# Performance work log

Measured on AMD Instinct MI355X. Metric: run time of the kernel, lower is better.

## Reference

```python
import jax, jax.numpy as jnp
import numpy as np

HIDDEN = 1024
NUM_HEADS = 16
HEAD_DIM = HIDDEN // NUM_HEADS


def setup_inputs() -> dict:
    key = jax.random.key(0)
    ks = jax.random.split(key, 9)
    B, S, Hs = 2, 2048, HIDDEN
    scale = 1.0 / np.sqrt(Hs)
    inp = {
        "hidden_state": jax.random.normal(ks[0], (B, S, Hs), dtype=jnp.float32),
        # causal mask, exactly (B, num_heads, S, S) as the module's assert requires
        "attention_mask": jnp.broadcast_to(
            jnp.tril(jnp.ones((S, S), dtype=bool)), (B, NUM_HEADS, S, S)
        ),
        "wq": jax.random.normal(ks[1], (Hs, Hs), dtype=jnp.float32) * scale,
        "bq": jnp.zeros((Hs,), dtype=jnp.float32),
        "wk": jax.random.normal(ks[2], (Hs, Hs), dtype=jnp.float32) * scale,
        "bk": jnp.zeros((Hs,), dtype=jnp.float32),
        "wv": jax.random.normal(ks[3], (Hs, Hs), dtype=jnp.float32) * scale,
        "bv": jnp.zeros((Hs,), dtype=jnp.float32),
        "wo": jax.random.normal(ks[4], (Hs, Hs), dtype=jnp.float32) * scale,
        "bo": jnp.zeros((Hs,), dtype=jnp.float32),
    }
    return inp


def _split_heads(x):
    B, S, _ = x.shape
    return x.reshape(B, S, NUM_HEADS, HEAD_DIM).transpose(0, 2, 1, 3)  # (B,H,S,D)


def reference(hidden_state, attention_mask, wq, bq, wk, bk, wv, bv, wo, bo):
    B, S, Hs = hidden_state.shape
    # torch nn.Linear: x @ W.T + b
    q = _split_heads(hidden_state @ wq.T + bq)
    k = _split_heads(hidden_state @ wk.T + bk)
    v = _split_heads(hidden_state @ wv.T + bv)
    scores = jnp.einsum("bhsd,bhtd->bhst", q, k) / jnp.sqrt(
        jnp.asarray(HEAD_DIM, dtype=jnp.float32)
    )
    scores = jnp.where(attention_mask, scores, -jnp.inf)
    probs = jax.nn.softmax(scores, axis=-1)
    # dropout p=0.0 (eval/deterministic) -> identity
    out = jnp.einsum("bhst,bhtd->bhsd", probs, v)
    out = out.transpose(0, 2, 1, 3).reshape(B, S, Hs)
    return out @ wo.T + bo
```

## Files before the change

### kernel.cpp

```cpp
#include <hip/hip_runtime.h>
#include <stdint.h>
#include <stddef.h>


typedef __attribute__((ext_vector_type(8))) short short8;
typedef __attribute__((ext_vector_type(4))) float f32x4;
typedef __attribute__((ext_vector_type(4))) unsigned int u32x4;
typedef __attribute__((ext_vector_type(2))) unsigned int u32x2;
typedef __attribute__((ext_vector_type(4))) unsigned short u16x4;

static __device__ __forceinline__ unsigned short f2bf(float f){
  union { float f; unsigned u; } v; v.f = f;
  unsigned r = v.u + 0x7FFFu + ((v.u >> 16) & 1u);
  return (unsigned short)(r >> 16);
}
static __device__ __forceinline__ unsigned pk2bf(float lo, float hi){
  return (unsigned)f2bf(lo) | ((unsigned)f2bf(hi) << 16);
}

static __device__ __forceinline__ void gl_lds16(const void* g, void* l){
  __builtin_amdgcn_global_load_lds((const __attribute__((address_space(1))) void*)g,
                                   (__attribute__((address_space(3))) void*)l, 16, 0, 0);
}

__global__ __launch_bounds__(256) void k_cvt_all(const float* __restrict__ X,
                                                 const float* __restrict__ w0, const float* __restrict__ w1,
                                                 const float* __restrict__ w2, const float* __restrict__ w3,
                                                 unsigned short* __restrict__ Xb,
                                                 unsigned short* __restrict__ Wb){
  int bid = blockIdx.x;
  const float* src; unsigned short* dst; int i;
  if (bid < 4096){ src = X; dst = Xb; i = bid*256 + threadIdx.x; }
  else {
    int w = (bid - 4096) >> 10;
    const float* srcs[4] = {w0,w1,w2,w3};
    src = srcs[w]; dst = Wb + (size_t)w*1048576u;
    i = ((bid - 4096) & 1023)*256 + threadIdx.x;
  }
  f32x4 x = ((const f32x4*)src)[i];
  u16x4 y = { f2bf(x[0]), f2bf(x[1]), f2bf(x[2]), f2bf(x[3]) };
  ((u16x4*)dst)[i] = y;
}

template<int MODE, int MT>
__global__ __launch_bounds__(256) void k_gemm_bt(
    const unsigned short* __restrict__ A,
    const unsigned short* __restrict__ B,
    const float* __restrict__ bias0, const float* __restrict__ bias1, const float* __restrict__ bias2,
    void* __restrict__ Cout, unsigned short* __restrict__ Vt, int N, int K)
{
  static_assert(MT==64 || MT==128, "MT");
  constexpr int I  = MT/32;
  constexpr int NA = MT/64;
  __shared__ unsigned short lds_a[MT*32];
  __shared__ unsigned short lds_b[128*32];
  const int t = threadIdx.x;
  const int lane = t & 63, wave = t >> 6;
  const int wy = wave >> 1, wx = wave & 1;
  const int m0 = blockIdx.y * MT, n0 = blockIdx.x * 128;
  const int mrow = lane & 15, quad = lane >> 4;
  const unsigned short* ga = A + (size_t)(m0 + (t>>2)) * K + (t&3)*8;
  const unsigned short* gb = B + (size_t)(n0 + (t>>2)) * K + (t&3)*8;
  char* la = (char*)lds_a + wave*1024;
  char* lb = (char*)lds_b + wave*1024;

  f32x4 acc[I][4];
  #pragma unroll
  for (int i=0;i<I;i++)
    #pragma unroll
    for (int j=0;j<4;j++) acc[i][j] = (f32x4){0.f,0.f,0.f,0.f};

  for (int k0=0;k0<K;k0+=32){
    __syncthreads();
    #pragma unroll
    for (int p=0;p<NA;p++) gl_lds16(ga + (size_t)p*64*K + k0, la + p*4096);
    #pragma unroll
    for (int p=0;p<2;p++)  gl_lds16(gb + (size_t)p*64*K + k0, lb + p*4096);
    __syncthreads();
    short8 af[I], bf[4];
    #pragma unroll
    for (int i=0;i<I;i++) af[i] = *(const short8*)(lds_a + (wy*(MT/2)+i*16+mrow)*32 + quad*8);
    #pragma unroll
    for (int j=0;j<4;j++) bf[j] = *(const short8*)(lds_b + (wx*64+j*16+mrow)*32 + quad*8);
    #pragma unroll
    for (int i=0;i<I;i++)
      #pragma unroll
      for (int j=0;j<4;j++)
        acc[i][j] = __builtin_amdgcn_mfma_f32_16x16x32_bf16(af[i], bf[j], acc[i][j], 0,0,0);
  }

  const bool vblk = (MODE==0) && (n0 >= 2048);
  #pragma unroll
  for (int j=0;j<4;j++){
    int col = n0 + wx*64 + j*16 + mrow;
    float bv;
    if (MODE==0){
      int cb = col >> 10;
      const float* bp = (cb==0)?bias0:((cb==1)?bias1:bias2);
      bv = bp[col & 1023];
    } else {
      bv = bias0[col];
    }
    #pragma unroll
    for (int i=0;i<I;i++){
      int rbase = m0 + wy*(MT/2) + i*16 + quad*4;
      if (vblk){
        int bh = (rbase >> 11) * 16 + ((col >> 6) & 15);
        unsigned short* vp = Vt + ((size_t)bh*64 + (col & 63))*2048 + (rbase & 2047);
        u32x2 w = { pk2bf(acc[i][0 ][0], 0.f) };
        (void)w;
        u32x2 wv = { pk2bf(acc[i][j][0]+bv, acc[i][j][1]+bv),
                     pk2bf(acc[i][j][2]+bv, acc[i][j][3]+bv) };
        *(u32x2*)vp = wv;
      } else {
        #pragma unroll
        for (int r=0;r<4;r++){
          float v = acc[i][j][r] + bv;
          if (MODE==1) ((float*)Cout)[(size_t)(rbase+r)*N + col] = v;
          else         ((unsigned short*)Cout)[(size_t)(rbase+r)*N + col] = f2bf(v);
        }
      }
    }
  }
}

__global__ __launch_bounds__(256) void k_attn(const unsigned short* __restrict__ QKV,
                                              const unsigned short* __restrict__ Vt,
                                              unsigned short* __restrict__ Ctx){
  __shared__ unsigned short lds_k[64*72];
  __shared__ unsigned short lds_v[64*72];
  __shared__ unsigned short lds_p[4][16*72];
  const int t = threadIdx.x;
  const int lane = t & 63, wave = t >> 6;
  const int mrow = lane & 15, quad = lane >> 4;
  const int bh = blockIdx.y, b = bh >> 4, h = bh & 15;
  const int qt = (bh & 16) ? (15 - blockIdx.x) : blockIdx.x;
  const int q0 = qt * 128;
  const size_t qkvbase = (size_t)b*2048*3072 + (size_t)h*64;
  const float C1 = 0.125f * 1.44269504f;
  const float C0 = -16.f  * 1.44269504f;

  short8 qf[2][2];
  #pragma unroll
  for (int qh=0;qh<2;qh++){
    const unsigned short* qp = QKV + qkvbase + (size_t)(q0 + qh*64 + wave*16 + mrow) * 3072;
    qf[qh][0] = *(const short8*)(qp + quad*8);
    qf[qh][1] = *(const short8*)(qp + 32 + quad*8);
  }
  float l_i[2] = {0.f, 0.f};
  f32x4 oacc[2][4];
  #pragma unroll
  for (int qh=0;qh<2;qh++)
    #pragma unroll
    for (int c=0;c<4;c++) oacc[qh][c] = (f32x4){0.f,0.f,0.f,0.f};

  const int njt = 2*qt + 2;
  const unsigned short* kbase = QKV + qkvbase + 1024;
  const unsigned short* vbase = Vt + (size_t)bh*64*2048;
  const int sr = t >> 3, sc = (t & 7) * 8;

  for (int jt=0;jt<njt;jt++){
    const int j0 = jt*64;
    __syncthreads();
    #pragma unroll
    for (int p=0;p<2;p++){
      int r = sr + p*32;
      *(u32x4*)(lds_k + r*72 + sc) = *(const u32x4*)(kbase + (size_t)(j0+r)*3072 + sc);
      *(u32x4*)(lds_v + r*72 + sc) = *(const u32x4*)(vbase + (size_t)r*2048 + j0 + sc);
    }
    __syncthreads();

    #pragma unroll
    for (int qh=0;qh<2;qh++){
      if (qh==0 && jt==njt-1) continue;
      const int grow = q0 + qh*64 + wave*16 + mrow;

      f32x4 sacc[4];
      #pragma unroll
      for (int jb=0;jb<4;jb++) sacc[jb] = (f32x4){0.f,0.f,0.f,0.f};
      #pragma unroll
      for (int jb=0;jb<4;jb++)
        #pragma unroll
        for (int kk=0;kk<2;kk++){
          short8 kf = *(const short8*)(lds_k + (jb*16+mrow)*72 + kk*32 + quad*8);
          sacc[jb] = __builtin_amdgcn_mfma_f32_16x16x32_bf16(kf, qf[qh][kk], sacc[jb], 0,0,0);
        }

      float s[4][4];
      if (jt == 2*qt + qh){
        #pragma unroll
        for (int jb=0;jb<4;jb++){
          int jg = j0 + jb*16 + quad*4;
          #pragma unroll
          for (int r=0;r<4;r++){
            float v = fmaf(sacc[jb][r], C1, C0);
            s[jb][r] = __builtin_amdgcn_exp2f((jg + r <= grow) ? v : -1e30f);
          }
        }
      } else {
        #pragma unroll
        for (int jb=0;jb<4;jb++)
          #pragma unroll
          for (int r=0;r<4;r++)
            s[jb][r] = __builtin_amdgcn_exp2f(fmaf(sacc[jb][r], C1, C0));
      }
      #pragma unroll
      for (int jb=0;jb<4;jb++)
        #pragma unroll
        for (int r=0;r<4;r++) l_i[qh] += s[jb][r];

      unsigned short* pp = lds_p[wave];
      #pragma unroll
      for (int jb=0;jb<4;jb++){
        u32x2 w = { pk2bf(s[jb][0], s[jb][1]), pk2bf(s[jb][2], s[jb][3]) };
        *(u32x2*)(pp + mrow*72 + jb*16 + quad*4) = w;
      }
      __asm__ volatile("s_waitcnt lgkmcnt(0)" ::: "memory");
      short8 pf[2];
      pf[0] = *(const short8*)(pp + mrow*72 + quad*8);
      pf[1] = *(const short8*)(pp + mrow*72 + 32 + quad*8);

      #pragma unroll
      for (int c=0;c<4;c++)
        #pragma unroll
        for (int kk=0;kk<2;kk++){
          short8 vf = *(const short8*)(lds_v + (c*16+mrow)*72 + kk*32 + quad*8);
          oacc[qh][c] = __builtin_amdgcn_mfma_f32_16x16x32_bf16(vf, pf[kk], oacc[qh][c], 0,0,0);
        }
    }
  }

  unsigned short* cp = Ctx + (size_t)b*2048*1024 + (size_t)h*64;
  #pragma unroll
  for (int qh=0;qh<2;qh++){
    float l = l_i[qh];
    l += __shfl_xor(l, 16);
    l += __shfl_xor(l, 32);
    float rl = 1.f / l;
    size_t rowoff = (size_t)(q0 + qh*64 + wave*16 + mrow) * 1024;
    #pragma unroll
    for (int c=0;c<4;c++){
      u32x2 w = { pk2bf(oacc[qh][c][0]*rl, oacc[qh][c][1]*rl),
                  pk2bf(oacc[qh][c][2]*rl, oacc[qh][c][3]*rl) };
      *(u32x2*)(cp + rowoff + c*16 + quad*4) = w;
    }
  }
}

extern "C" void kernel_launch(void* const* d_in, const int* in_sizes, int n_in,
                              void* d_out, int out_size, void* d_ws, size_t ws_size,
                              hipStream_t stream){
  const float* X  = (const float*)d_in[0];
  const float* wq = (const float*)d_in[2];
  const float* bq = (const float*)d_in[3];
  const float* wk = (const float*)d_in[4];
  const float* bk = (const float*)d_in[5];
  const float* wv = (const float*)d_in[6];
  const float* bv = (const float*)d_in[7];
  const float* wo = (const float*)d_in[8];
  const float* bo = (const float*)d_in[9];

  char* ws = (char*)d_ws;
  unsigned short* Xb   = (unsigned short*)(ws);
  unsigned short* Wb   = (unsigned short*)(ws + (8u<<20));
  unsigned short* QKVb = (unsigned short*)(ws + (16u<<20));
  unsigned short* Vt   = (unsigned short*)(ws + (40u<<20));
  unsigned short* Ctxb = (unsigned short*)(ws + (48u<<20));

  k_cvt_all<<<dim3(8192), 256, 0, stream>>>(X, wq, wk, wv, wo, Xb, Wb);
  k_gemm_bt<0,128><<<dim3(24, 32), 256, 0, stream>>>(Xb, Wb, bq, bk, bv, QKVb, Vt, 3072, 1024);
  k_attn<<<dim3(16, 32), 256, 0, stream>>>(QKVb, Vt, Ctxb);
  k_gemm_bt<1,64><<<dim3(8, 64), 256, 0, stream>>>(Ctxb, Wb + 3u*1048576u, bo, bo, bo,
                                                   d_out, nullptr, 1024, 1024);
}
```

Measured before the change: 714.7 us.

## Double-buffer K/V tiles and split query halves across 8 waves in attention

```diff
diff --git a/kernel.cpp b/kernel.cpp
--- a/kernel.cpp
+++ b/kernel.cpp
@@ -107,8 +107,6 @@
       if (vblk){
         int bh = (rbase >> 11) * 16 + ((col >> 6) & 15);
         unsigned short* vp = Vt + ((size_t)bh*64 + (col & 63))*2048 + (rbase & 2047);
-        u32x2 w = { pk2bf(acc[i][0 ][0], 0.f) };
-        (void)w;
         u32x2 wv = { pk2bf(acc[i][j][0]+bv, acc[i][j][1]+bv),
                      pk2bf(acc[i][j][2]+bv, acc[i][j][3]+bv) };
         *(u32x2*)vp = wv;
@@ -124,15 +122,16 @@
   }
 }
 
-__global__ __launch_bounds__(256) void k_attn(const unsigned short* __restrict__ QKV,
-                                              const unsigned short* __restrict__ Vt,
-                                              unsigned short* __restrict__ Ctx){
-  __shared__ unsigned short lds_k[64*72];
-  __shared__ unsigned short lds_v[64*72];
-  __shared__ unsigned short lds_p[4][16*72];
+__global__ __launch_bounds__(512, 4) void k_attn(const unsigned short* __restrict__ QKV,
+                                                 const unsigned short* __restrict__ Vt,
+                                                 unsigned short* __restrict__ Ctx){
+  __shared__ unsigned short lds_k[2][64*72];
+  __shared__ unsigned short lds_v[2][64*72];
+  __shared__ unsigned short lds_p[8][16*72];
   const int t = threadIdx.x;
   const int lane = t & 63, wave = t >> 6;
   const int mrow = lane & 15, quad = lane >> 4;
+  const int qh = wave >> 2;
   const int bh = blockIdx.y, b = bh >> 4, h = bh & 15;
   const int qt = (bh & 16) ? (15 - blockIdx.x) : blockIdx.x;
   const int q0 = qt * 128;
@@ -140,40 +139,44 @@
   const float C1 = 0.125f * 1.44269504f;
   const float C0 = -16.f  * 1.44269504f;
 
-  short8 qf[2][2];
+  const int grow = q0 + wave*16 + mrow;
+  short8 qf[2];
+  {
+    const unsigned short* qp = QKV + qkvbase + (size_t)grow * 3072;
+    qf[0] = *(const short8*)(qp + quad*8);
+    qf[1] = *(const short8*)(qp + 32 + quad*8);
+  }
+  float l_i = 0.f;
+  f32x4 oacc[4];
   #pragma unroll
-  for (int qh=0;qh<2;qh++){
-    const unsigned short* qp = QKV + qkvbase + (size_t)(q0 + qh*64 + wave*16 + mrow) * 3072;
-    qf[qh][0] = *(const short8*)(qp + quad*8);
-    qf[qh][1] = *(const short8*)(qp + 32 + quad*8);
-  }
-  float l_i[2] = {0.f, 0.f};
-  f32x4 oacc[2][4];
-  #pragma unroll
-  for (int qh=0;qh<2;qh++)
-    #pragma unroll
-    for (int c=0;c<4;c++) oacc[qh][c] = (f32x4){0.f,0.f,0.f,0.f};
+  for (int c=0;c<4;c++) oacc[c] = (f32x4){0.f,0.f,0.f,0.f};
 
   const int njt = 2*qt + 2;
+  const int mask_jt = 2*qt + qh;
+  const int skip_jt = (qh==0) ? (njt-1) : -1;
   const unsigned short* kbase = QKV + qkvbase + 1024;
   const unsigned short* vbase = Vt + (size_t)bh*64*2048;
   const int sr = t >> 3, sc = (t & 7) * 8;
 
+  u32x4 kreg = *(const u32x4*)(kbase + (size_t)sr*3072 + sc);
+  u32x4 vreg = *(const u32x4*)(vbase + (size_t)sr*2048 + sc);
+  *(u32x4*)(&lds_k[0][0] + sr*72 + sc) = kreg;
+  *(u32x4*)(&lds_v[0][0] + sr*72 + sc) = vreg;
+
+  int buf = 0;
   for (int jt=0;jt<njt;jt++){
-    const int j0 = jt*64;
     __syncthreads();
-    #pragma unroll
-    for (int p=0;p<2;p++){
-      int r = sr + p*32;
-      *(u32x4*)(lds_k + r*72 + sc) = *(const u32x4*)(kbase + (size_t)(j0+r)*3072 + sc);
-      *(u32x4*)(lds_v + r*72 + sc) = *(const u32x4*)(vbase + (size_t)r*2048 + j0 + sc);
-    }
-    __syncthreads();
-
-    #pragma unroll
-    for (int qh=0;qh<2;qh++){
-      if (qh==0 && jt==njt-1) continue;
-      const int grow = q0 + qh*64 + wave*16 + mrow;
+
+    {
+      const int pj = (jt+1 < njt) ? (jt+1)*64 : 0;
+      kreg = *(const u32x4*)(kbase + (size_t)(pj+sr)*3072 + sc);
+      vreg = *(const u32x4*)(vbase + (size_t)sr*2048 + pj + sc);
+    }
+
+    if (jt != skip_jt){
+      const int j0 = jt*64;
+      const unsigned short* lk = &lds_k[buf][0];
+      const unsigned short* lv = &lds_v[buf][0];
 
       f32x4 sacc[4];
       #pragma unroll
@@ -182,12 +185,12 @@
       for (int jb=0;jb<4;jb++)
         #pragma unroll
         for (int kk=0;kk<2;kk++){
-          short8 kf = *(const short8*)(lds_k + (jb*16+mrow)*72 + kk*32 + quad*8);
-          sacc[jb] = __builtin_amdgcn_mfma_f32_16x16x32_bf16(kf, qf[qh][kk], sacc[jb], 0,0,0);
+          short8 kf = *(const short8*)(lk + (jb*16+mrow)*72 + kk*32 + quad*8);
+          sacc[jb] = __builtin_amdgcn_mfma_f32_16x16x32_bf16(kf, qf[kk], sacc[jb], 0,0,0);
         }
 
       float s[4][4];
-      if (jt == 2*qt + qh){
+      if (jt == mask_jt){
         #pragma unroll
         for (int jb=0;jb<4;jb++){
           int jg = j0 + jb*16 + quad*4;
@@ -207,7 +210,7 @@
       #pragma unroll
       for (int jb=0;jb<4;jb++)
         #pragma unroll
-        for (int r=0;r<4;r++) l_i[qh] += s[jb][r];
+        for (int r=0;r<4;r++) l_i += s[jb][r];
 
       unsigned short* pp = lds_p[wave];
       #pragma unroll
@@ -224,24 +227,27 @@
       for (int c=0;c<4;c++)
         #pragma unroll
         for (int kk=0;kk<2;kk++){
-          short8 vf = *(const short8*)(lds_v + (c*16+mrow)*72 + kk*32 + quad*8);
-          oacc[qh][c] = __builtin_amdgcn_mfma_f32_16x16x32_bf16(vf, pf[kk], oacc[qh][c], 0,0,0);
-        }
-    }
+          short8 vf = *(const short8*)(lv + (c*16+mrow)*72 + kk*32 + quad*8);
+          oacc[c] = __builtin_amdgcn_mfma_f32_16x16x32_bf16(vf, pf[kk], oacc[c], 0,0,0);
+        }
+    }
+
+    *(u32x4*)(&lds_k[buf^1][0] + sr*72 + sc) = kreg;
+    *(u32x4*)(&lds_v[buf^1][0] + sr*72 + sc) = vreg;
+    buf ^= 1;
   }
 
   unsigned short* cp = Ctx + (size_t)b*2048*1024 + (size_t)h*64;
-  #pragma unroll
-  for (int qh=0;qh<2;qh++){
-    float l = l_i[qh];
+  {
+    float l = l_i;
     l += __shfl_xor(l, 16);
     l += __shfl_xor(l, 32);
     float rl = 1.f / l;
-    size_t rowoff = (size_t)(q0 + qh*64 + wave*16 + mrow) * 1024;
+    size_t rowoff = (size_t)grow * 1024;
     #pragma unroll
     for (int c=0;c<4;c++){
-      u32x2 w = { pk2bf(oacc[qh][c][0]*rl, oacc[qh][c][1]*rl),
-                  pk2bf(oacc[qh][c][2]*rl, oacc[qh][c][3]*rl) };
+      u32x2 w = { pk2bf(oacc[c][0]*rl, oacc[c][1]*rl),
+                  pk2bf(oacc[c][2]*rl, oacc[c][3]*rl) };
       *(u32x2*)(cp + rowoff + c*16 + quad*4) = w;
     }
   }
@@ -269,7 +275,7 @@
 
   k_cvt_all<<<dim3(8192), 256, 0, stream>>>(X, wq, wk, wv, wo, Xb, Wb);
   k_gemm_bt<0,128><<<dim3(24, 32), 256, 0, stream>>>(Xb, Wb, bq, bk, bv, QKVb, Vt, 3072, 1024);
-  k_attn<<<dim3(16, 32), 256, 0, stream>>>(QKVb, Vt, Ctxb);
+  k_attn<<<dim3(16, 32), 512, 0, stream>>>(QKVb, Vt, Ctxb);
   k_gemm_bt<1,64><<<dim3(8, 64), 256, 0, stream>>>(Ctxb, Wb + 3u*1048576u, bo, bo, bo,
                                                    d_out, nullptr, 1024, 1024);
 }
```

Result: faster. 696.7 us (-2.5%).

## Double-buffer K/V tiles in attention, keep P in registers, skip masked blocks

Applied to the files above, without the earlier changes.

```diff
diff --git a/kernel.cpp b/kernel.cpp
--- a/kernel.cpp
+++ b/kernel.cpp
@@ -4,11 +4,20 @@
 
 
 typedef __attribute__((ext_vector_type(8))) short short8;
+typedef __attribute__((ext_vector_type(4))) short bf16x4;
 typedef __attribute__((ext_vector_type(4))) float f32x4;
 typedef __attribute__((ext_vector_type(4))) unsigned int u32x4;
 typedef __attribute__((ext_vector_type(2))) unsigned int u32x2;
 typedef __attribute__((ext_vector_type(4))) unsigned short u16x4;
 
+#if __has_builtin(__builtin_amdgcn_mfma_f32_16x16x16bf16_1k)
+  #define MFMA16(a,b,c) __builtin_amdgcn_mfma_f32_16x16x16bf16_1k(a,b,c,0,0,0)
+#elif __has_builtin(__builtin_amdgcn_mfma_f32_16x16x16_bf16)
+  #define MFMA16(a,b,c) __builtin_amdgcn_mfma_f32_16x16x16_bf16(a,b,c,0,0,0)
+#else
+  #define MFMA16(a,b,c) (c)
+#endif
+
 static __device__ __forceinline__ unsigned short f2bf(float f){
   union { float f; unsigned u; } v; v.f = f;
   unsigned r = v.u + 0x7FFFu + ((v.u >> 16) & 1u);
@@ -16,6 +25,11 @@
 }
 static __device__ __forceinline__ unsigned pk2bf(float lo, float hi){
   return (unsigned)f2bf(lo) | ((unsigned)f2bf(hi) << 16);
+}
+static __device__ __forceinline__ unsigned pk2bf_hw(float lo, float hi){
+  unsigned r;
+  asm("v_cvt_pk_bf16_f32 %0, %1, %2" : "=v"(r) : "v"(lo), "v"(hi));
+  return r;
 }
 
 static __device__ __forceinline__ void gl_lds16(const void* g, void* l){
@@ -107,8 +121,6 @@
       if (vblk){
         int bh = (rbase >> 11) * 16 + ((col >> 6) & 15);
         unsigned short* vp = Vt + ((size_t)bh*64 + (col & 63))*2048 + (rbase & 2047);
-        u32x2 w = { pk2bf(acc[i][0 ][0], 0.f) };
-        (void)w;
         u32x2 wv = { pk2bf(acc[i][j][0]+bv, acc[i][j][1]+bv),
                      pk2bf(acc[i][j][2]+bv, acc[i][j][3]+bv) };
         *(u32x2*)vp = wv;
@@ -124,12 +136,11 @@
   }
 }
 
-__global__ __launch_bounds__(256) void k_attn(const unsigned short* __restrict__ QKV,
-                                              const unsigned short* __restrict__ Vt,
-                                              unsigned short* __restrict__ Ctx){
-  __shared__ unsigned short lds_k[64*72];
-  __shared__ unsigned short lds_v[64*72];
-  __shared__ unsigned short lds_p[4][16*72];
+__global__ __launch_bounds__(256, 2) void k_attn(const unsigned short* __restrict__ QKV,
+                                                 const unsigned short* __restrict__ Vt,
+                                                 unsigned short* __restrict__ Ctx){
+  __shared__ unsigned short lds_k[2][128*72];
+  __shared__ unsigned short lds_v[2][64*136];
   const int t = threadIdx.x;
   const int lane = t & 63, wave = t >> 6;
   const int mrow = lane & 15, quad = lane >> 4;
@@ -140,10 +151,11 @@
   const float C1 = 0.125f * 1.44269504f;
   const float C0 = -16.f  * 1.44269504f;
 
-  short8 qf[2][2];
+  int grow2[2]; short8 qf[2][2];
   #pragma unroll
   for (int qh=0;qh<2;qh++){
-    const unsigned short* qp = QKV + qkvbase + (size_t)(q0 + qh*64 + wave*16 + mrow) * 3072;
+    grow2[qh] = q0 + wave*32 + qh*16 + mrow;
+    const unsigned short* qp = QKV + qkvbase + (size_t)grow2[qh] * 3072;
     qf[qh][0] = *(const short8*)(qp + quad*8);
     qf[qh][1] = *(const short8*)(qp + 32 + quad*8);
   }
@@ -154,80 +166,109 @@
     #pragma unroll
     for (int c=0;c<4;c++) oacc[qh][c] = (f32x4){0.f,0.f,0.f,0.f};
 
-  const int njt = 2*qt + 2;
+  const int njt = qt + 1;
   const unsigned short* kbase = QKV + qkvbase + 1024;
   const unsigned short* vbase = Vt + (size_t)bh*64*2048;
-  const int sr = t >> 3, sc = (t & 7) * 8;
-
+
+  u32x4 kreg[4], vreg[4];
+  #pragma unroll
+  for (int p=0;p<4;p++){
+    int c = t + 256*p;
+    kreg[p] = *(const u32x4*)(kbase + (size_t)(c>>3)*3072 + (c&7)*8);
+    vreg[p] = *(const u32x4*)(vbase + (size_t)(c>>4)*2048 + (c&15)*8);
+  }
+  #pragma unroll
+  for (int p=0;p<4;p++){
+    int c = t + 256*p;
+    *(u32x4*)(&lds_k[0][0] + (c>>3)*72  + (c&7)*8)  = kreg[p];
+    *(u32x4*)(&lds_v[0][0] + (c>>4)*136 + (c&15)*8) = vreg[p];
+  }
+
+  int buf = 0;
   for (int jt=0;jt<njt;jt++){
-    const int j0 = jt*64;
     __syncthreads();
-    #pragma unroll
-    for (int p=0;p<2;p++){
-      int r = sr + p*32;
-      *(u32x4*)(lds_k + r*72 + sc) = *(const u32x4*)(kbase + (size_t)(j0+r)*3072 + sc);
-      *(u32x4*)(lds_v + r*72 + sc) = *(const u32x4*)(vbase + (size_t)r*2048 + j0 + sc);
-    }
-    __syncthreads();
-
+
+    {
+      const int pj = (jt+1 < njt) ? (jt+1)*128 : 0;
+      #pragma unroll
+      for (int p=0;p<4;p++){
+        int c = t + 256*p;
+        kreg[p] = *(const u32x4*)(kbase + (size_t)(pj + (c>>3))*3072 + (c&7)*8);
+        vreg[p] = *(const u32x4*)(vbase + (size_t)(c>>4)*2048 + pj + (c&15)*8);
+      }
+    }
+
+    const int j0 = jt*128;
+    const bool diag = (jt == qt);
+    const unsigned short* lk = &lds_k[buf][0];
+    const unsigned short* lv = &lds_v[buf][0];
+
+    f32x4 sacc[2][8];
+    __builtin_amdgcn_s_setprio(1);
+    #pragma unroll
+    for (int jb=0;jb<8;jb++){
+      if (diag && jb > 2*wave+1) continue;
+      short8 kf0 = *(const short8*)(lk + (jb*16+mrow)*72 + quad*8);
+      short8 kf1 = *(const short8*)(lk + (jb*16+mrow)*72 + 32 + quad*8);
+      #pragma unroll
+      for (int qh=0;qh<2;qh++){
+        if (diag && jb > 2*wave+qh) continue;
+        f32x4 a = (f32x4){0.f,0.f,0.f,0.f};
+        a = __builtin_amdgcn_mfma_f32_16x16x32_bf16(kf0, qf[qh][0], a, 0,0,0);
+        a = __builtin_amdgcn_mfma_f32_16x16x32_bf16(kf1, qf[qh][1], a, 0,0,0);
+        sacc[qh][jb] = a;
+      }
+    }
+    __builtin_amdgcn_s_setprio(0);
+
+    unsigned puv[2][8][2];
     #pragma unroll
     for (int qh=0;qh<2;qh++){
-      if (qh==0 && jt==njt-1) continue;
-      const int grow = q0 + qh*64 + wave*16 + mrow;
-
-      f32x4 sacc[4];
-      #pragma unroll
-      for (int jb=0;jb<4;jb++) sacc[jb] = (f32x4){0.f,0.f,0.f,0.f};
-      #pragma unroll
-      for (int jb=0;jb<4;jb++)
+      #pragma unroll
+      for (int jb=0;jb<8;jb++){
+        if (diag && jb > 2*wave+qh) continue;
+        float v[4];
         #pragma unroll
-        for (int kk=0;kk<2;kk++){
-          short8 kf = *(const short8*)(lds_k + (jb*16+mrow)*72 + kk*32 + quad*8);
-          sacc[jb] = __builtin_amdgcn_mfma_f32_16x16x32_bf16(kf, qf[qh][kk], sacc[jb], 0,0,0);
+        for (int r=0;r<4;r++){
+          float x = fmaf(sacc[qh][jb][r], C1, C0);
+          if (diag){
+            int jg = j0 + jb*16 + quad*4 + r;
+            x = (jg <= grow2[qh]) ? x : -1e30f;
+          }
+          v[r] = __builtin_amdgcn_exp2f(x);
         }
-
-      float s[4][4];
-      if (jt == 2*qt + qh){
+        l_i[qh] += v[0]+v[1]+v[2]+v[3];
+        puv[qh][jb][0] = pk2bf_hw(v[0], v[1]);
+        puv[qh][jb][1] = pk2bf_hw(v[2], v[3]);
+      }
+    }
+
+    __builtin_amdgcn_s_setprio(1);
+    #pragma unroll
+    for (int jb=0;jb<8;jb++){
+      if (diag && jb > 2*wave+1) continue;
+      #pragma unroll
+      for (int c=0;c<4;c++){
+        bf16x4 vfr = *(const bf16x4*)(lv + (c*16+mrow)*136 + jb*16 + quad*4);
         #pragma unroll
-        for (int jb=0;jb<4;jb++){
-          int jg = j0 + jb*16 + quad*4;
-          #pragma unroll
-          for (int r=0;r<4;r++){
-            float v = fmaf(sacc[jb][r], C1, C0);
-            s[jb][r] = __builtin_amdgcn_exp2f((jg + r <= grow) ? v : -1e30f);
-          }
+        for (int qh=0;qh<2;qh++){
+          if (diag && jb > 2*wave+qh) continue;
+          union { unsigned u[2]; bf16x4 s4; } pw;
+          pw.u[0] = puv[qh][jb][0];
+          pw.u[1] = puv[qh][jb][1];
+          oacc[qh][c] = MFMA16(vfr, pw.s4, oacc[qh][c]);
         }
-      } else {
-        #pragma unroll
-        for (int jb=0;jb<4;jb++)
-          #pragma unroll
-          for (int r=0;r<4;r++)
-            s[jb][r] = __builtin_amdgcn_exp2f(fmaf(sacc[jb][r], C1, C0));
-      }
-      #pragma unroll
-      for (int jb=0;jb<4;jb++)
-        #pragma unroll
-        for (int r=0;r<4;r++) l_i[qh] += s[jb][r];
-
-      unsigned short* pp = lds_p[wave];
-      #pragma unroll
-      for (int jb=0;jb<4;jb++){
-        u32x2 w = { pk2bf(s[jb][0], s[jb][1]), pk2bf(s[jb][2], s[jb][3]) };
-        *(u32x2*)(pp + mrow*72 + jb*16 + quad*4) = w;
-      }
-      __asm__ volatile("s_waitcnt lgkmcnt(0)" ::: "memory");
-      short8 pf[2];
-      pf[0] = *(const short8*)(pp + mrow*72 + quad*8);
-      pf[1] = *(const short8*)(pp + mrow*72 + 32 + quad*8);
-
-      #pragma unroll
-      for (int c=0;c<4;c++)
-        #pragma unroll
-        for (int kk=0;kk<2;kk++){
-          short8 vf = *(const short8*)(lds_v + (c*16+mrow)*72 + kk*32 + quad*8);
-          oacc[qh][c] = __builtin_amdgcn_mfma_f32_16x16x32_bf16(vf, pf[kk], oacc[qh][c], 0,0,0);
-        }
-    }
+      }
+    }
+    __builtin_amdgcn_s_setprio(0);
+
+    #pragma unroll
+    for (int p=0;p<4;p++){
+      int c = t + 256*p;
+      *(u32x4*)(&lds_k[buf^1][0] + (c>>3)*72  + (c&7)*8)  = kreg[p];
+      *(u32x4*)(&lds_v[buf^1][0] + (c>>4)*136 + (c&15)*8) = vreg[p];
+    }
+    buf ^= 1;
   }
 
   unsigned short* cp = Ctx + (size_t)b*2048*1024 + (size_t)h*64;
@@ -237,7 +278,7 @@
     l += __shfl_xor(l, 16);
     l += __shfl_xor(l, 32);
     float rl = 1.f / l;
-    size_t rowoff = (size_t)(q0 + qh*64 + wave*16 + mrow) * 1024;
+    size_t rowoff = (size_t)grow2[qh] * 1024;
     #pragma unroll
     for (int c=0;c<4;c++){
       u32x2 w = { pk2bf(oacc[qh][c][0]*rl, oacc[qh][c][1]*rl),
```

Result: faster. 695.2 us (-2.7%).
